# Performance work log

Measured on AMD Instinct MI355X. Metric: run time of the kernel, lower is better.

The kernel has to match this reference:

```python
import jax, jax.numpy as jnp
import numpy as np

N = 50000
E = 800000
D_IN, D_HID, D_OUT = 256, 512, 256
LN_EPS = 1e-5


def setup_inputs() -> dict:
    key = jax.random.key(0)
    ks = jax.random.split(key, 8)
    return {
        "v": jax.random.normal(ks[0], (N, D_IN), dtype=jnp.float32),
        "edge_weight": jax.random.uniform(ks[1], (E,), dtype=jnp.float32),
        "epsilon": jnp.zeros((1, 1), dtype=jnp.float32),
        "w1": jax.random.normal(ks[2], (D_HID, D_IN), dtype=jnp.float32) * (1.0 / np.sqrt(D_IN)),
        "b1": jnp.zeros((D_HID,), dtype=jnp.float32),
        "g1": jnp.ones((D_HID,), dtype=jnp.float32),
        "beta1": jnp.zeros((D_HID,), dtype=jnp.float32),
        "w2": jax.random.normal(ks[3], (D_OUT, D_HID), dtype=jnp.float32) * (1.0 / np.sqrt(D_HID)),
        "b2": jnp.zeros((D_OUT,), dtype=jnp.float32),
        "g2": jnp.ones((D_OUT,), dtype=jnp.float32),
        "beta2": jnp.zeros((D_OUT,), dtype=jnp.float32),
        "src": jax.random.randint(ks[4], (E,), 0, N, dtype=jnp.int32),
        "dst": jax.random.randint(ks[5], (E,), 0, N, dtype=jnp.int32),
    }


def _layer_norm(x, g, b):
    mu = jnp.mean(x, axis=-1, keepdims=True)
    var = jnp.mean(jnp.square(x - mu), axis=-1, keepdims=True)
    return (x - mu) * jax.lax.rsqrt(var + LN_EPS) * g + b


def reference(v, edge_weight, epsilon, w1, b1, g1, beta1, w2, b2, g2, beta2, src, dst):
    # sparse adjacency aggregation: agg[dst] += w * v[src]   (torch.sparse.mm(a, v))
    msgs = v[src] * edge_weight[:, None]            # [E, D_IN]
    agg = jax.ops.segment_sum(msgs, dst, num_segments=v.shape[0])  # [N, D_IN]
    h = agg + epsilon * v                            # epsilon residual
    # MLP: Linear -> LayerNorm -> ReLU  (x2)
    h = jax.nn.relu(_layer_norm(h @ w1.T + b1, g1, beta1))
    h = jax.nn.relu(_layer_norm(h @ w2.T + b2, g2, beta2))
    return h
```

## Files before the change

kernel.cpp:

```cpp
#include <hip/hip_runtime.h>

#define D_IN 256
#define D_HID 512
#define D_OUT 256
#define LN_EPS 1e-5f
#define SCAN_B 512

typedef __attribute__((ext_vector_type(8))) short bf16x8;
typedef __attribute__((ext_vector_type(4))) float f32x4;

__device__ __forceinline__ ushort f2bf(float x) {
    union { float f; unsigned u; } c; c.f = x;
    unsigned r = c.u + 0x7FFFu + ((c.u >> 16) & 1u);
    return (ushort)(r >> 16);
}
__device__ __forceinline__ float bf2f(unsigned b) {
    union { unsigned u; float f; } c; c.u = b << 16;
    return c.f;
}

__global__ void prep_kernel(const float* __restrict__ v, const float* __restrict__ w1,
                            const float* __restrict__ w2, ushort* __restrict__ vb,
                            ushort* __restrict__ w1b, ushort* __restrict__ w2b,
                            int* __restrict__ cnt, int n4v, int nzero,
                            int bv, int bw) {
    int b = blockIdx.x, t = threadIdx.x;
    if (b < bv) {
        int i = b * 256 + t;
        if (i < n4v) {
            float4 x = ((const float4*)v)[i];
            ((ushort4*)vb)[i] = make_ushort4(f2bf(x.x), f2bf(x.y), f2bf(x.z), f2bf(x.w));
        }
    } else if (b < bv + bw) {
        int j = (b - bv) * 256 + t;
        if (j < 32768) {
            float4 x = ((const float4*)w1)[j];
            ((ushort4*)w1b)[j] = make_ushort4(f2bf(x.x), f2bf(x.y), f2bf(x.z), f2bf(x.w));
        } else {
            int k = j - 32768;
            float4 x = ((const float4*)w2)[k];
            ((ushort4*)w2b)[k] = make_ushort4(f2bf(x.x), f2bf(x.y), f2bf(x.z), f2bf(x.w));
        }
    } else {
        int i = (b - bv - bw) * 256 + t;
        if (i < nzero) cnt[i] = 0;
    }
}

__global__ void hist_kernel(const int* __restrict__ dst, int* __restrict__ cnt, int E) {
    int e = blockIdx.x * 256 + threadIdx.x;
    if (e < E) atomicAdd(&cnt[dst[e]], 1);
}

__global__ __launch_bounds__(SCAN_B) void scan1_kernel(const int* __restrict__ cnt,
                                                       int* __restrict__ offs,
                                                       int* __restrict__ bsum, int n) {
    __shared__ int s[SCAN_B];
    int i = blockIdx.x * SCAN_B + threadIdx.x;
    int x = (i < n) ? cnt[i] : 0;
    s[threadIdx.x] = x;
    __syncthreads();
    for (int o = 1; o < SCAN_B; o <<= 1) {
        int t = (threadIdx.x >= (unsigned)o) ? s[threadIdx.x - o] : 0;
        __syncthreads();
        s[threadIdx.x] += t;
        __syncthreads();
    }
    if (i < n) offs[i] = s[threadIdx.x] - x;
    if (threadIdx.x == SCAN_B - 1) bsum[blockIdx.x] = s[threadIdx.x];
}

__global__ __launch_bounds__(SCAN_B) void scan3_kernel(int* __restrict__ offs,
                                                       int* __restrict__ cursor,
                                                       const int* __restrict__ bsum,
                                                       int n, int E, int nb) {
    __shared__ int s[SCAN_B];
    int t = threadIdx.x;
    s[t] = (t < nb && t < (int)blockIdx.x) ? bsum[t] : 0;
    __syncthreads();
    for (int o = SCAN_B / 2; o > 0; o >>= 1) {
        if (t < o) s[t] += s[t + o];
        __syncthreads();
    }
    int base = s[0];
    int i = blockIdx.x * SCAN_B + t;
    if (i < n) {
        int v0 = offs[i] + base;
        offs[i] = v0;
        cursor[i] = v0;
    }
    if (i == 0) offs[n] = E;
}

__global__ void fill_kernel(const int* __restrict__ src, const int* __restrict__ dst,
                            const float* __restrict__ ew, int* __restrict__ cursor,
                            int2* __restrict__ perm, int E) {
    int e = blockIdx.x * 256 + threadIdx.x;
    if (e >= E) return;
    int p = atomicAdd(&cursor[dst[e]], 1);
    perm[p] = make_int2(src[e], __float_as_int(ew[e]));
}

__global__ __launch_bounds__(256) void aggregate_kernel(
    const ushort* __restrict__ vb, const float* __restrict__ eps_p,
    const int* __restrict__ offs, const int2* __restrict__ perm,
    ushort* __restrict__ aggb, int N) {
    int node = blockIdx.x * 4 + (threadIdx.x >> 6);
    if (node >= N) return;
    int lane = threadIdx.x & 63;
    int beg = offs[node], end = offs[node + 1];
    float a0 = 0.f, a1 = 0.f, a2 = 0.f, a3 = 0.f;
    float c0 = 0.f, c1 = 0.f, c2 = 0.f, c3 = 0.f;

    int i = beg;
    for (; i + 8 <= end; i += 8) {
        int2 p0 = perm[i + 0], p1 = perm[i + 1], p2 = perm[i + 2], p3 = perm[i + 3];
        int2 p4 = perm[i + 4], p5 = perm[i + 5], p6 = perm[i + 6], p7 = perm[i + 7];
        float w0 = __int_as_float(p0.y), w1 = __int_as_float(p1.y);
        float w2 = __int_as_float(p2.y), w3 = __int_as_float(p3.y);
        float w4 = __int_as_float(p4.y), w5 = __int_as_float(p5.y);
        float w6 = __int_as_float(p6.y), w7 = __int_as_float(p7.y);
        ushort4 r0 = ((const ushort4*)(vb + (size_t)p0.x * D_IN))[lane];
        ushort4 r1 = ((const ushort4*)(vb + (size_t)p1.x * D_IN))[lane];
        ushort4 r2 = ((const ushort4*)(vb + (size_t)p2.x * D_IN))[lane];
        ushort4 r3 = ((const ushort4*)(vb + (size_t)p3.x * D_IN))[lane];
        ushort4 r4 = ((const ushort4*)(vb + (size_t)p4.x * D_IN))[lane];
        ushort4 r5 = ((const ushort4*)(vb + (size_t)p5.x * D_IN))[lane];
        ushort4 r6 = ((const ushort4*)(vb + (size_t)p6.x * D_IN))[lane];
        ushort4 r7 = ((const ushort4*)(vb + (size_t)p7.x * D_IN))[lane];
        a0 += w0 * bf2f(r0.x) + w1 * bf2f(r1.x) + w2 * bf2f(r2.x) + w3 * bf2f(r3.x);
        a1 += w0 * bf2f(r0.y) + w1 * bf2f(r1.y) + w2 * bf2f(r2.y) + w3 * bf2f(r3.y);
        a2 += w0 * bf2f(r0.z) + w1 * bf2f(r1.z) + w2 * bf2f(r2.z) + w3 * bf2f(r3.z);
        a3 += w0 * bf2f(r0.w) + w1 * bf2f(r1.w) + w2 * bf2f(r2.w) + w3 * bf2f(r3.w);
        c0 += w4 * bf2f(r4.x) + w5 * bf2f(r5.x) + w6 * bf2f(r6.x) + w7 * bf2f(r7.x);
        c1 += w4 * bf2f(r4.y) + w5 * bf2f(r5.y) + w6 * bf2f(r6.y) + w7 * bf2f(r7.y);
        c2 += w4 * bf2f(r4.z) + w5 * bf2f(r5.z) + w6 * bf2f(r6.z) + w7 * bf2f(r7.z);
        c3 += w4 * bf2f(r4.w) + w5 * bf2f(r5.w) + w6 * bf2f(r6.w) + w7 * bf2f(r7.w);
    }
    for (; i + 4 <= end; i += 4) {
        int2 p0 = perm[i + 0], p1 = perm[i + 1], p2 = perm[i + 2], p3 = perm[i + 3];
        float w0 = __int_as_float(p0.y), w1 = __int_as_float(p1.y);
        float w2 = __int_as_float(p2.y), w3 = __int_as_float(p3.y);
        ushort4 r0 = ((const ushort4*)(vb + (size_t)p0.x * D_IN))[lane];
        ushort4 r1 = ((const ushort4*)(vb + (size_t)p1.x * D_IN))[lane];
        ushort4 r2 = ((const ushort4*)(vb + (size_t)p2.x * D_IN))[lane];
        ushort4 r3 = ((const ushort4*)(vb + (size_t)p3.x * D_IN))[lane];
        a0 += w0 * bf2f(r0.x) + w1 * bf2f(r1.x) + w2 * bf2f(r2.x) + w3 * bf2f(r3.x);
        a1 += w0 * bf2f(r0.y) + w1 * bf2f(r1.y) + w2 * bf2f(r2.y) + w3 * bf2f(r3.y);
        a2 += w0 * bf2f(r0.z) + w1 * bf2f(r1.z) + w2 * bf2f(r2.z) + w3 * bf2f(r3.z);
        a3 += w0 * bf2f(r0.w) + w1 * bf2f(r1.w) + w2 * bf2f(r2.w) + w3 * bf2f(r3.w);
    }
    for (; i < end; ++i) {
        int2 p = perm[i];
        float w = __int_as_float(p.y);
        ushort4 r = ((const ushort4*)(vb + (size_t)p.x * D_IN))[lane];
        a0 += w * bf2f(r.x); a1 += w * bf2f(r.y);
        a2 += w * bf2f(r.z); a3 += w * bf2f(r.w);
    }
    a0 += c0; a1 += c1; a2 += c2; a3 += c3;
    float eps = eps_p[0];
    ushort4 m = ((const ushort4*)(vb + (size_t)node * D_IN))[lane];
    a0 += eps * bf2f(m.x); a1 += eps * bf2f(m.y);
    a2 += eps * bf2f(m.z); a3 += eps * bf2f(m.w);
    ((ushort4*)(aggb + (size_t)node * D_IN))[lane] =
        make_ushort4(f2bf(a0), f2bf(a1), f2bf(a2), f2bf(a3));
}

#define BS1_OFF 2048
#define BS2_OFF 32768
#define HS_IDX(row, col) ((row) * 512 + ((col) ^ (((row) & 7) << 3)))

__global__ __launch_bounds__(256, 2) void mlp_kernel(
    const ushort* __restrict__ A, const ushort* __restrict__ w1b,
    const ushort* __restrict__ w2b,
    const float* __restrict__ b1, const float* __restrict__ g1, const float* __restrict__ be1,
    const float* __restrict__ b2, const float* __restrict__ g2, const float* __restrict__ be2,
    float* __restrict__ out, int N) {
    __shared__ ushort lds[40960];
    float* redf = (float*)&lds[BS2_OFF];

    int t = threadIdx.x;
    int w = t >> 6, lane = t & 63;
    int row0 = blockIdx.x * 64;
    int fr = lane & 15, q = lane >> 4, kb = q * 8;
    int lrow = lane >> 2, lcol = (lane & 3) * 8;

    f32x4 acc[4][8];
    #pragma unroll
    for (int m = 0; m < 4; ++m)
        #pragma unroll
        for (int c = 0; c < 8; ++c) {
            f32x4 z = {0.f, 0.f, 0.f, 0.f};
            acc[m][c] = z;
        }

    for (int k0 = 0; k0 < D_IN; k0 += 32) {
        {
            int ar = row0 + w * 16 + lrow;
            if (ar > N - 1) ar = N - 1;
            const ushort* gp = A + (size_t)ar * D_IN + k0 + lcol;
            __builtin_amdgcn_global_load_lds(
                (const __attribute__((address_space(1))) void*)gp,
                (__attribute__((address_space(3))) void*)(&lds[(w * 16) * 32]),
                16, 0, 0);
        }
        #pragma unroll
        for (int c = 0; c < 8; ++c) {
            int br = w * 128 + c * 16 + lrow;
            const ushort* gp = w1b + (size_t)br * D_IN + k0 + lcol;
            __builtin_amdgcn_global_load_lds(
                (const __attribute__((address_space(1))) void*)gp,
                (__attribute__((address_space(3))) void*)(&lds[BS1_OFF + (w * 128 + c * 16) * 32]),
                16, 0, 0);
        }
        __syncthreads();

        bf16x8 af[4], bf[8];
        #pragma unroll
        for (int m = 0; m < 4; ++m)
            af[m] = *(const bf16x8*)&lds[(m * 16 + fr) * 32 + kb];
        #pragma unroll
        for (int c = 0; c < 8; ++c)
            bf[c] = *(const bf16x8*)&lds[BS1_OFF + (w * 128 + c * 16 + fr) * 32 + kb];
        #pragma unroll
        for (int m = 0; m < 4; ++m)
            #pragma unroll
            for (int c = 0; c < 8; ++c)
                acc[m][c] = __builtin_amdgcn_mfma_f32_16x16x32_bf16(af[m], bf[c], acc[m][c], 0, 0, 0);
        __syncthreads();
    }

    {
        float bi[8], gg[8], bb[8];
        #pragma unroll
        for (int c = 0; c < 8; ++c) {
            int col = w * 128 + c * 16 + fr;
            bi[c] = b1[col]; gg[c] = g1[col]; bb[c] = be1[col];
        }
        #pragma unroll
        for (int m = 0; m < 4; ++m) {
            #pragma unroll
            for (int r = 0; r < 4; ++r) {
                float s = 0.f, sq = 0.f;
                #pragma unroll
                for (int c = 0; c < 8; ++c) {
                    float x = acc[m][c][r] + bi[c];
                    acc[m][c][r] = x;
                    s += x; sq += x * x;
                }
                #pragma unroll
                for (int o = 1; o < 16; o <<= 1) {
                    s  += __shfl_xor(s, o, 64);
                    sq += __shfl_xor(sq, o, 64);
                }
                if (fr == 0) {
                    int row = m * 16 + q * 4 + r;
                    redf[row * 4 + w]       = s;
                    redf[256 + row * 4 + w] = sq;
                }
            }
        }
        __syncthreads();
        if (t < 64) {
            float s  = redf[t * 4 + 0] + redf[t * 4 + 1] + redf[t * 4 + 2] + redf[t * 4 + 3];
            float sq = redf[256 + t * 4 + 0] + redf[256 + t * 4 + 1] +
                       redf[256 + t * 4 + 2] + redf[256 + t * 4 + 3];
            float mu = s / (float)D_HID;
            float var = sq / (float)D_HID - mu * mu;
            redf[512 + t] = mu;
            redf[576 + t] = rsqrtf(var + LN_EPS);
        }
        __syncthreads();
        #pragma unroll
        for (int m = 0; m < 4; ++m) {
            #pragma unroll
            for (int r = 0; r < 4; ++r) {
                int row = m * 16 + q * 4 + r;
                float mu = redf[512 + row], rs = redf[576 + row];
                #pragma unroll
                for (int c = 0; c < 8; ++c) {
                    int col = w * 128 + c * 16 + fr;
                    float y = (acc[m][c][r] - mu) * rs * gg[c] + bb[c];
                    lds[HS_IDX(row, col)] = f2bf(fmaxf(y, 0.f));
                }
            }
        }
    }
    __syncthreads();

    f32x4 acc2[4][4];
    #pragma unroll
    for (int m = 0; m < 4; ++m)
        #pragma unroll
        for (int c = 0; c < 4; ++c) {
            f32x4 z = {0.f, 0.f, 0.f, 0.f};
            acc2[m][c] = z;
        }

    for (int k0 = 0; k0 < D_HID; k0 += 32) {
        #pragma unroll
        for (int c = 0; c < 4; ++c) {
            int br = w * 64 + c * 16 + lrow;
            const ushort* gp = w2b + (size_t)br * D_HID + k0 + lcol;
            __builtin_amdgcn_global_load_lds(
                (const __attribute__((address_space(1))) void*)gp,
                (__attribute__((address_space(3))) void*)(&lds[BS2_OFF + (w * 64 + c * 16) * 32]),
                16, 0, 0);
        }
        __syncthreads();

        bf16x8 af[4], bf[4];
        #pragma unroll
        for (int m = 0; m < 4; ++m) {
            int row = m * 16 + fr;
            af[m] = *(const bf16x8*)&lds[HS_IDX(row, k0 + kb)];
        }
        #pragma unroll
        for (int c = 0; c < 4; ++c)
            bf[c] = *(const bf16x8*)&lds[BS2_OFF + (w * 64 + c * 16 + fr) * 32 + kb];
        #pragma unroll
        for (int m = 0; m < 4; ++m)
            #pragma unroll
            for (int c = 0; c < 4; ++c)
                acc2[m][c] = __builtin_amdgcn_mfma_f32_16x16x32_bf16(af[m], bf[c], acc2[m][c], 0, 0, 0);
        __syncthreads();
    }

    {
        float bi[4], gg[4], bb[4];
        #pragma unroll
        for (int c = 0; c < 4; ++c) {
            int col = w * 64 + c * 16 + fr;
            bi[c] = b2[col]; gg[c] = g2[col]; bb[c] = be2[col];
        }
        #pragma unroll
        for (int m = 0; m < 4; ++m) {
            #pragma unroll
            for (int r = 0; r < 4; ++r) {
                float s = 0.f, sq = 0.f;
                #pragma unroll
                for (int c = 0; c < 4; ++c) {
                    float x = acc2[m][c][r] + bi[c];
                    acc2[m][c][r] = x;
                    s += x; sq += x * x;
                }
                #pragma unroll
                for (int o = 1; o < 16; o <<= 1) {
                    s  += __shfl_xor(s, o, 64);
                    sq += __shfl_xor(sq, o, 64);
                }
                if (fr == 0) {
                    int row = m * 16 + q * 4 + r;
                    redf[row * 4 + w]       = s;
                    redf[256 + row * 4 + w] = sq;
                }
            }
        }
        __syncthreads();
        if (t < 64) {
            float s  = redf[t * 4 + 0] + redf[t * 4 + 1] + redf[t * 4 + 2] + redf[t * 4 + 3];
            float sq = redf[256 + t * 4 + 0] + redf[256 + t * 4 + 1] +
                       redf[256 + t * 4 + 2] + redf[256 + t * 4 + 3];
            float mu = s / (float)D_OUT;
            float var = sq / (float)D_OUT - mu * mu;
            redf[512 + t] = mu;
            redf[576 + t] = rsqrtf(var + LN_EPS);
        }
        __syncthreads();
        #pragma unroll
        for (int m = 0; m < 4; ++m) {
            #pragma unroll
            for (int r = 0; r < 4; ++r) {
                int row = m * 16 + q * 4 + r;
                int grow = row0 + row;
                if (grow >= N) continue;
                float mu = redf[512 + row], rs = redf[576 + row];
                #pragma unroll
                for (int c = 0; c < 4; ++c) {
                    int col = w * 64 + c * 16 + fr;
                    float y = (acc2[m][c][r] - mu) * rs * gg[c] + bb[c];
                    out[(size_t)grow * D_OUT + col] = fmaxf(y, 0.f);
                }
            }
        }
    }
}

extern "C" void kernel_launch(void* const* d_in, const int* in_sizes, int n_in,
                              void* d_out, int out_size, void* d_ws, size_t ws_size,
                              hipStream_t stream) {
    const float* v     = (const float*)d_in[0];
    const float* ew    = (const float*)d_in[1];
    const float* eps   = (const float*)d_in[2];
    const float* w1    = (const float*)d_in[3];
    const float* b1    = (const float*)d_in[4];
    const float* g1    = (const float*)d_in[5];
    const float* beta1 = (const float*)d_in[6];
    const float* w2    = (const float*)d_in[7];
    const float* b2    = (const float*)d_in[8];
    const float* g2    = (const float*)d_in[9];
    const float* beta2 = (const float*)d_in[10];
    const int*   src   = (const int*)d_in[11];
    const int*   dst   = (const int*)d_in[12];

    int N = in_sizes[0] / D_IN;
    int E = in_sizes[1];

    float* out = (float*)d_out;

    char* ws = (char*)d_ws;
    size_t off = 0;
    ushort* vb   = (ushort*)(ws + off); off += (size_t)N * D_IN * 2;
    ushort* aggb = (ushort*)(ws + off); off += (size_t)N * D_IN * 2;
    ushort* w1b  = (ushort*)(ws + off); off += (size_t)D_HID * D_IN * 2;
    ushort* w2b  = (ushort*)(ws + off); off += (size_t)D_OUT * D_HID * 2;
    int* offs     = (int*)(ws + off); off += (size_t)(N + 256) * 4;
    int* cursor   = (int*)(ws + off); off += (size_t)(N + 256) * 4;
    int* bsum     = (int*)(ws + off); off += 1024;
    int2* perm    = (int2*)(ws + off); off += (size_t)E * 8;

    int nb = (N + SCAN_B - 1) / SCAN_B;
    int n4v = N * (D_IN / 4);
    int bv = (n4v + 255) / 256;
    int bw = 256;
    int bz = (N + 255) / 256;

    prep_kernel<<<bv + bw + bz, 256, 0, stream>>>(v, w1, w2, vb, w1b, w2b,
                                                  cursor, n4v, N, bv, bw);

    hist_kernel<<<(E + 255) / 256, 256, 0, stream>>>(dst, cursor, E);
    scan1_kernel<<<nb, SCAN_B, 0, stream>>>(cursor, offs, bsum, N);
    scan3_kernel<<<nb, SCAN_B, 0, stream>>>(offs, cursor, bsum, N, E, nb);
    fill_kernel<<<(E + 255) / 256, 256, 0, stream>>>(src, dst, ew, cursor, perm, E);

    aggregate_kernel<<<(N + 3) / 4, 256, 0, stream>>>(vb, eps, offs, perm, aggb, N);

    int mblocks = (N + 63) / 64;
    mlp_kernel<<<mblocks, 256, 0, stream>>>(aggb, w1b, w2b,
                                            b1, g1, beta1, b2, g2, beta2, out, N);
}
```

Before: 332.4 us.

## Load MLP GEMM operands directly from global memory instead of LDS staging

Both GEMM loops in the fused MLP kernel stop staging A, W1 and W2 tiles in LDS through global_load_lds. Each wave now reads its MFMA fragments straight from global memory (the weights are expected to be cache-resident), which removes the per-iteration barriers and LDS traffic. LDS is split into a dedicated hidden-activation buffer and a reduction buffer. The cost is redundant global reads, since the A rows are loaded by all four waves, and uncoalesced 16-byte row-strided loads with no software prefetch.

Result: slower. 360.9 us (+8.6%).

```diff
diff --git a/kernel.cpp b/kernel.cpp
--- a/kernel.cpp
+++ b/kernel.cpp
@@ -166,8 +166,6 @@
         make_ushort4(f2bf(a0), f2bf(a1), f2bf(a2), f2bf(a3));
 }
 
-#define BS1_OFF 2048
-#define BS2_OFF 32768
 #define HS_IDX(row, col) ((row) * 512 + ((col) ^ (((row) & 7) << 3)))
 
 __global__ __launch_bounds__(256, 2) void mlp_kernel(
@@ -176,14 +174,21 @@
     const float* __restrict__ b1, const float* __restrict__ g1, const float* __restrict__ be1,
     const float* __restrict__ b2, const float* __restrict__ g2, const float* __restrict__ be2,
     float* __restrict__ out, int N) {
-    __shared__ ushort lds[40960];
-    float* redf = (float*)&lds[BS2_OFF];
+    __shared__ ushort hs[32768];
+    __shared__ float redf[640];
 
     int t = threadIdx.x;
     int w = t >> 6, lane = t & 63;
     int row0 = blockIdx.x * 64;
     int fr = lane & 15, q = lane >> 4, kb = q * 8;
-    int lrow = lane >> 2, lcol = (lane & 3) * 8;
+
+    int arow[4];
+    #pragma unroll
+    for (int m = 0; m < 4; ++m) {
+        int ar = row0 + m * 16 + fr;
+        if (ar > N - 1) ar = N - 1;
+        arow[m] = ar;
+    }
 
     f32x4 acc[4][8];
     #pragma unroll
@@ -195,39 +200,18 @@
         }
 
     for (int k0 = 0; k0 < D_IN; k0 += 32) {
-        {
-            int ar = row0 + w * 16 + lrow;
-            if (ar > N - 1) ar = N - 1;
-            const ushort* gp = A + (size_t)ar * D_IN + k0 + lcol;
-            __builtin_amdgcn_global_load_lds(
-                (const __attribute__((address_space(1))) void*)gp,
-                (__attribute__((address_space(3))) void*)(&lds[(w * 16) * 32]),
-                16, 0, 0);
-        }
-        #pragma unroll
-        for (int c = 0; c < 8; ++c) {
-            int br = w * 128 + c * 16 + lrow;
-            const ushort* gp = w1b + (size_t)br * D_IN + k0 + lcol;
-            __builtin_amdgcn_global_load_lds(
-                (const __attribute__((address_space(1))) void*)gp,
-                (__attribute__((address_space(3))) void*)(&lds[BS1_OFF + (w * 128 + c * 16) * 32]),
-                16, 0, 0);
-        }
-        __syncthreads();
-
         bf16x8 af[4], bf[8];
         #pragma unroll
         for (int m = 0; m < 4; ++m)
-            af[m] = *(const bf16x8*)&lds[(m * 16 + fr) * 32 + kb];
+            af[m] = *(const bf16x8*)(A + (size_t)arow[m] * D_IN + k0 + kb);
         #pragma unroll
         for (int c = 0; c < 8; ++c)
-            bf[c] = *(const bf16x8*)&lds[BS1_OFF + (w * 128 + c * 16 + fr) * 32 + kb];
+            bf[c] = *(const bf16x8*)(w1b + (size_t)(w * 128 + c * 16 + fr) * D_IN + k0 + kb);
         #pragma unroll
         for (int m = 0; m < 4; ++m)
             #pragma unroll
             for (int c = 0; c < 8; ++c)
                 acc[m][c] = __builtin_amdgcn_mfma_f32_16x16x32_bf16(af[m], bf[c], acc[m][c], 0, 0, 0);
-        __syncthreads();
     }
 
     {
@@ -281,7 +265,7 @@
                 for (int c = 0; c < 8; ++c) {
                     int col = w * 128 + c * 16 + fr;
                     float y = (acc[m][c][r] - mu) * rs * gg[c] + bb[c];
-                    lds[HS_IDX(row, col)] = f2bf(fmaxf(y, 0.f));
+                    hs[HS_IDX(row, col)] = f2bf(fmaxf(y, 0.f));
                 }
             }
         }
@@ -298,32 +282,18 @@
         }
 
     for (int k0 = 0; k0 < D_HID; k0 += 32) {
-        #pragma unroll
-        for (int c = 0; c < 4; ++c) {
-            int br = w * 64 + c * 16 + lrow;
-            const ushort* gp = w2b + (size_t)br * D_HID + k0 + lcol;
-            __builtin_amdgcn_global_load_lds(
-                (const __attribute__((address_space(1))) void*)gp,
-                (__attribute__((address_space(3))) void*)(&lds[BS2_OFF + (w * 64 + c * 16) * 32]),
-                16, 0, 0);
-        }
-        __syncthreads();
-
-        bf16x8 af[4], bf[4];
-        #pragma unroll
-        for (int m = 0; m < 4; ++m) {
-            int row = m * 16 + fr;
-            af[m] = *(const bf16x8*)&lds[HS_IDX(row, k0 + kb)];
-        }
+        bf16x8 af2[4], bf2[4];
+        #pragma unroll
+        for (int m = 0; m < 4; ++m)
+            af2[m] = *(const bf16x8*)&hs[HS_IDX(m * 16 + fr, k0 + kb)];
         #pragma unroll
         for (int c = 0; c < 4; ++c)
-            bf[c] = *(const bf16x8*)&lds[BS2_OFF + (w * 64 + c * 16 + fr) * 32 + kb];
+            bf2[c] = *(const bf16x8*)(w2b + (size_t)(w * 64 + c * 16 + fr) * D_HID + k0 + kb);
         #pragma unroll
         for (int m = 0; m < 4; ++m)
             #pragma unroll
             for (int c = 0; c < 4; ++c)
-                acc2[m][c] = __builtin_amdgcn_mfma_f32_16x16x32_bf16(af[m], bf[c], acc2[m][c], 0, 0, 0);
-        __syncthreads();
+                acc2[m][c] = __builtin_amdgcn_mfma_f32_16x16x32_bf16(af2[m], bf2[c], acc2[m][c], 0, 0, 0);
     }
 
     {
```
